# Kernel optimization log

Hardware: AMD Instinct MI355X
Metric: run time of the kernel (lower is better)

Reference implementation:

```python
import jax, jax.numpy as jnp
import numpy as np


def _square_distance(src, dst):
    # src: [B,N,C], dst: [B,M,C] -> [B,N,M] squared euclidean distances
    # ||s-d||^2 = -2 s.d + ||s||^2 + ||d||^2
    d = -2.0 * jnp.einsum('bnc,bmc->bnm', src, dst)
    d = d + jnp.sum(src * src, axis=-1)[:, :, None]
    d = d + jnp.sum(dst * dst, axis=-1)[:, None, :]
    return d


def setup_inputs() -> dict:
    key = jax.random.key(0)
    k1, k2 = jax.random.split(key)
    B, N, M, C = 8, 4096, 4096, 3
    f = jax.random.normal(k1, (B, N, C), dtype=jnp.float32)
    f_ = jax.random.normal(k2, (B, M, C), dtype=jnp.float32)
    return {"f": f, "f_": f_}


def reference(f, f_):
    dis = _square_distance(f, f_)          # [B,N,M]
    f2f_ = jnp.min(dis, axis=2)            # [B,N] nearest in f_ for each f point
    f_2f = jnp.min(dis, axis=1)            # [B,M] nearest in f for each f_ point
    d = jnp.mean(f2f_, axis=1) + jnp.mean(f_2f, axis=1)  # [B]
    return jnp.mean(d)
```

## Files before the change

### kernel.cpp

```cpp
#include <hip/hip_runtime.h>


typedef __attribute__((ext_vector_type(8))) short bf16x8;
typedef __attribute__((ext_vector_type(4))) float f32x4;

constexpr int B = 8;
constexpr int N = 4096;
constexpr int M = 4096;

constexpr int ROWS_PER_BLOCK = 128;
constexpr int SEG = 1024;
constexpr int SEGS = M / SEG;
constexpr int TILES = SEG / 16;

static __device__ __forceinline__ unsigned short f2bf(float v) {
    unsigned u = __float_as_uint(v);
    return (unsigned short)((u + 0x7FFFu + ((u >> 16) & 1u)) >> 16);
}
static __device__ __forceinline__ float bf2f(unsigned short b) {
    return __uint_as_float(((unsigned)b) << 16);
}
static __device__ __forceinline__ void split3(float v, unsigned short& a,
                                              unsigned short& b, unsigned short& c) {
    a = f2bf(v); float r = v - bf2f(a);
    b = f2bf(r); r -= bf2f(b);
    c = f2bf(r);
}

__global__ __launch_bounds__(256, 2) void chamfer_dir_mfma(
    const float* __restrict__ f,
    const float* __restrict__ f_,
    unsigned int* __restrict__ minA,
    unsigned int* __restrict__ minB)
{
    __shared__ bf16x8 Bt[TILES * 64];

    const int tid  = threadIdx.x;
    const int lane = tid & 63;
    const int w    = tid >> 6;
    const int r    = lane & 15;
    const int kg   = lane >> 4;

    const int dir = blockIdx.z;
    const int b   = blockIdx.y;
    const int rc  = blockIdx.x;

    const float* qsrc = dir ? f_ : f;
    const float* tsrc = dir ? f  : f_;
    unsigned int* omin = dir ? minB : minA;

    const int rowbase = rc * ROWS_PER_BLOCK + w * 32;
    bf16x8 afrag[2];
    #pragma unroll
    for (int rt = 0; rt < 2; ++rt) {
        const float* qp = qsrc + ((size_t)b * N + rowbase + rt * 16 + r) * 3;
        const float x = qp[0], y = qp[1], z = qp[2];
        unsigned short px0,px1,px2, py0,py1,py2, pz0,pz1,pz2, n0,n1,n2;
        split3(-2.f * x, px0, px1, px2);
        split3(-2.f * y, py0, py1, py2);
        split3(-2.f * z, pz0, pz1, pz2);
        split3(x*x + y*y + z*z, n0, n1, n2);
        const short ONE = 0x3F80;
        bf16x8 a;
        if (kg == 0)
            a = (bf16x8){(short)px0,(short)px0,(short)px1,(short)px1,(short)px0,(short)px2,(short)py0,(short)py0};
        else if (kg == 1)
            a = (bf16x8){(short)py1,(short)py1,(short)py0,(short)py2,(short)pz0,(short)pz0,(short)pz1,(short)pz1};
        else if (kg == 2)
            a = (bf16x8){(short)pz0,(short)pz2,(short)n0,(short)n1,(short)n2,ONE,ONE,ONE};
        else
            a = (bf16x8){0,0,0,0,0,0,0,0};
        afrag[rt] = a;
    }

    float rm[2][4];
    #pragma unroll
    for (int j = 0; j < 4; ++j) { rm[0][j] = 3.402823466e+38f; rm[1][j] = 3.402823466e+38f; }

    const float* tb = tsrc + (size_t)b * M * 3;
    const f32x4 zero = {0.f, 0.f, 0.f, 0.f};

    for (int s = 0; s < SEGS; ++s) {
        __syncthreads();
        #pragma unroll
        for (int i = 0; i < 4; ++i) {
            const int t = i * 256 + tid;
            const float* tp = tb + (size_t)(s * SEG + t) * 3;
            const float x = tp[0], y = tp[1], z = tp[2];
            unsigned short x0,x1,x2, y0,y1,y2, z0,z1,z2, m0,m1,m2;
            split3(x, x0, x1, x2);
            split3(y, y0, y1, y2);
            split3(z, z0, z1, z2);
            split3(x*x + y*y + z*z, m0, m1, m2);
            const short ONE = 0x3F80;
            const int tile = t >> 4, rr = t & 15;
            bf16x8* base = &Bt[tile * 64 + rr];
            base[ 0] = (bf16x8){(short)x0,(short)x1,(short)x0,(short)x1,(short)x2,(short)x0,(short)y0,(short)y1};
            base[16] = (bf16x8){(short)y0,(short)y1,(short)y2,(short)y0,(short)z0,(short)z1,(short)z0,(short)z1};
            base[32] = (bf16x8){(short)z2,(short)z0,ONE,ONE,ONE,(short)m0,(short)m1,(short)m2};
            base[48] = (bf16x8){0,0,0,0,0,0,0,0};
        }
        __syncthreads();

        bf16x8 bb = Bt[lane];
        #pragma unroll 4
        for (int ct = 0; ct < TILES; ++ct) {
            bf16x8 nb = Bt[((ct + 1) & (TILES - 1)) * 64 + lane];
            f32x4 c0 = __builtin_amdgcn_mfma_f32_16x16x32_bf16(afrag[0], bb, zero, 0, 0, 0);
            f32x4 c1 = __builtin_amdgcn_mfma_f32_16x16x32_bf16(afrag[1], bb, zero, 0, 0, 0);
            #pragma unroll
            for (int j = 0; j < 4; ++j) {
                rm[0][j] = fminf(rm[0][j], c0[j]);
                rm[1][j] = fminf(rm[1][j], c1[j]);
            }
            bb = nb;
        }
    }

    #pragma unroll
    for (int rt = 0; rt < 2; ++rt) {
        #pragma unroll
        for (int j = 0; j < 4; ++j) {
            float v = rm[rt][j];
            v = fminf(v, __shfl_xor(v, 1));
            v = fminf(v, __shfl_xor(v, 2));
            v = fminf(v, __shfl_xor(v, 4));
            v = fminf(v, __shfl_xor(v, 8));
            if (r == 0) {
                const int row = rowbase + rt * 16 + kg * 4 + j;
                atomicMin(&omin[b * N + row], __float_as_uint(v));
            }
        }
    }
}

__global__ __launch_bounds__(256) void reduce_out_kernel(
    const uint4* __restrict__ mins,
    float* __restrict__ out)
{
    __shared__ float wsum[4];
    const int tid = threadIdx.x;
    const uint4 v = mins[blockIdx.x * 256 + tid];
    float s = (__uint_as_float(v.x) + __uint_as_float(v.y))
            + (__uint_as_float(v.z) + __uint_as_float(v.w));

    #pragma unroll
    for (int off = 32; off > 0; off >>= 1) s += __shfl_down(s, off, 64);
    if ((tid & 63) == 0) wsum[tid >> 6] = s;
    __syncthreads();
    if (tid == 0) {
        const float r = (wsum[0] + wsum[1]) + (wsum[2] + wsum[3]);
        atomicAdd(out, r * (1.0f / 32768.0f));
    }
}

extern "C" void kernel_launch(void* const* d_in, const int* in_sizes, int n_in,
                              void* d_out, int out_size, void* d_ws, size_t ws_size,
                              hipStream_t stream) {
    (void)in_sizes; (void)n_in; (void)out_size; (void)ws_size;
    const float* f  = (const float*)d_in[0];
    const float* f_ = (const float*)d_in[1];
    float* out = (float*)d_out;

    unsigned int* minA = (unsigned int*)d_ws;
    unsigned int* minB = minA + (size_t)B * N;

    dim3 grid(N / ROWS_PER_BLOCK, B, 2);
    chamfer_dir_mfma<<<grid, 256, 0, stream>>>(f, f_, minA, minB);

    reduce_out_kernel<<<64, 256, 0, stream>>>((const uint4*)minA, out);
}
```

Before: 74.36 us.

## Precompute bf16 target fragments in a separate kernel and stream from global

Adds a prepass kernel that converts each target point into split-bf16 MFMA B-fragments once and stores them in workspace. The main kernel now reads these fragments straight from global memory, dropping the LDS staging and both per-segment barriers. It also splits the column range into four quarters per block, so the grid grows to 2048 blocks with a swizzled block index and higher occupancy. The trade-off is an extra launch, more global and L2 traffic for fragments, and four times as many atomicMin calls. Correctness depends on minA/minB being initialised elsewhere, as in the original code.

```diff
diff --git a/kernel.cpp b/kernel.cpp
--- a/kernel.cpp
+++ b/kernel.cpp
@@ -9,9 +9,9 @@
 constexpr int M = 4096;
 
 constexpr int ROWS_PER_BLOCK = 128;
-constexpr int SEG = 1024;
-constexpr int SEGS = M / SEG;
-constexpr int TILES = SEG / 16;
+constexpr int COLQ = 4;
+constexpr int CPB = M / COLQ;
+constexpr int TPB = CPB / 16;
 
 static __device__ __forceinline__ unsigned short f2bf(float v) {
     unsigned u = __float_as_uint(v);
@@ -27,13 +27,45 @@
     c = f2bf(r);
 }
 
-__global__ __launch_bounds__(256, 2) void chamfer_dir_mfma(
+__global__ __launch_bounds__(256) void make_frags(
     const float* __restrict__ f,
     const float* __restrict__ f_,
+    bf16x8* __restrict__ frag)
+{
+    const int gid = blockIdx.x * 256 + threadIdx.x;
+    const int dir = gid >> 15;
+    const int b   = (gid >> 12) & 7;
+    const int t   = gid & 4095;
+    const float* tsrc = dir ? f : f_;
+    const float* tp = tsrc + ((size_t)b * M + t) * 3;
+    const float x = tp[0], y = tp[1], z = tp[2];
+    unsigned short x0,x1,x2, y0,y1,y2, z0,z1,z2, m0,m1,m2;
+    split3(x, x0, x1, x2);
+    split3(y, y0, y1, y2);
+    split3(z, z0, z1, z2);
+    split3(x*x + y*y + z*z, m0, m1, m2);
+    const short ONE = 0x3F80;
+    const int tile = t >> 4, rr = t & 15;
+    bf16x8* base = frag + ((size_t)(dir * B + b) * 256 + tile) * 64 + rr;
+    base[ 0] = (bf16x8){(short)x0,(short)x1,(short)x0,(short)x1,(short)x2,(short)x0,(short)y0,(short)y1};
+    base[16] = (bf16x8){(short)y0,(short)y1,(short)y2,(short)y0,(short)z0,(short)z1,(short)z0,(short)z1};
+    base[32] = (bf16x8){(short)z2,(short)z0,ONE,ONE,ONE,(short)m0,(short)m1,(short)m2};
+    base[48] = (bf16x8){0,0,0,0,0,0,0,0};
+}
+
+__global__ __launch_bounds__(256, 6) void chamfer_dir_mfma(
+    const float* __restrict__ f,
+    const float* __restrict__ f_,
+    const bf16x8* __restrict__ frag,
     unsigned int* __restrict__ minA,
     unsigned int* __restrict__ minB)
 {
-    __shared__ bf16x8 Bt[TILES * 64];
+    const int bid = blockIdx.x;
+    const int swz = ((bid & 7) << 8) | (bid >> 3);
+    const int rc   = swz & 31;
+    const int cq   = (swz >> 5) & 3;
+    const int b    = (swz >> 7) & 7;
+    const int dir  = swz >> 10;
 
     const int tid  = threadIdx.x;
     const int lane = tid & 63;
@@ -41,12 +73,7 @@
     const int r    = lane & 15;
     const int kg   = lane >> 4;
 
-    const int dir = blockIdx.z;
-    const int b   = blockIdx.y;
-    const int rc  = blockIdx.x;
-
     const float* qsrc = dir ? f_ : f;
-    const float* tsrc = dir ? f  : f_;
     unsigned int* omin = dir ? minB : minA;
 
     const int rowbase = rc * ROWS_PER_BLOCK + w * 32;
@@ -77,44 +104,28 @@
     #pragma unroll
     for (int j = 0; j < 4; ++j) { rm[0][j] = 3.402823466e+38f; rm[1][j] = 3.402823466e+38f; }
 
-    const float* tb = tsrc + (size_t)b * M * 3;
+    const bf16x8* gf = frag + ((size_t)(dir * B + b) * 256 + cq * (TPB)) * 64;
     const f32x4 zero = {0.f, 0.f, 0.f, 0.f};
 
-    for (int s = 0; s < SEGS; ++s) {
-        __syncthreads();
+    bf16x8 bb0 = gf[lane];
+    bf16x8 bb1 = gf[64 + lane];
+    #pragma unroll 2
+    for (int it = 0; it < TPB / 2; ++it) {
+        bf16x8 nb0, nb1;
+        if (it + 1 < TPB / 2) {
+            nb0 = gf[(2 * it + 2) * 64 + lane];
+            nb1 = gf[(2 * it + 3) * 64 + lane];
+        }
+        f32x4 cA0 = __builtin_amdgcn_mfma_f32_16x16x32_bf16(afrag[0], bb0, zero, 0, 0, 0);
+        f32x4 cA1 = __builtin_amdgcn_mfma_f32_16x16x32_bf16(afrag[1], bb0, zero, 0, 0, 0);
+        f32x4 cB0 = __builtin_amdgcn_mfma_f32_16x16x32_bf16(afrag[0], bb1, zero, 0, 0, 0);
+        f32x4 cB1 = __builtin_amdgcn_mfma_f32_16x16x32_bf16(afrag[1], bb1, zero, 0, 0, 0);
         #pragma unroll
-        for (int i = 0; i < 4; ++i) {
-            const int t = i * 256 + tid;
-            const float* tp = tb + (size_t)(s * SEG + t) * 3;
-            const float x = tp[0], y = tp[1], z = tp[2];
-            unsigned short x0,x1,x2, y0,y1,y2, z0,z1,z2, m0,m1,m2;
-            split3(x, x0, x1, x2);
-            split3(y, y0, y1, y2);
-            split3(z, z0, z1, z2);
-            split3(x*x + y*y + z*z, m0, m1, m2);
-            const short ONE = 0x3F80;
-            const int tile = t >> 4, rr = t & 15;
-            bf16x8* base = &Bt[tile * 64 + rr];
-            base[ 0] = (bf16x8){(short)x0,(short)x1,(short)x0,(short)x1,(short)x2,(short)x0,(short)y0,(short)y1};
-            base[16] = (bf16x8){(short)y0,(short)y1,(short)y2,(short)y0,(short)z0,(short)z1,(short)z0,(short)z1};
-            base[32] = (bf16x8){(short)z2,(short)z0,ONE,ONE,ONE,(short)m0,(short)m1,(short)m2};
-            base[48] = (bf16x8){0,0,0,0,0,0,0,0};
+        for (int j = 0; j < 4; ++j) {
+            rm[0][j] = fminf(fminf(rm[0][j], cA0[j]), cB0[j]);
+            rm[1][j] = fminf(fminf(rm[1][j], cA1[j]), cB1[j]);
         }
-        __syncthreads();
-
-        bf16x8 bb = Bt[lane];
-        #pragma unroll 4
-        for (int ct = 0; ct < TILES; ++ct) {
-            bf16x8 nb = Bt[((ct + 1) & (TILES - 1)) * 64 + lane];
-            f32x4 c0 = __builtin_amdgcn_mfma_f32_16x16x32_bf16(afrag[0], bb, zero, 0, 0, 0);
-            f32x4 c1 = __builtin_amdgcn_mfma_f32_16x16x32_bf16(afrag[1], bb, zero, 0, 0, 0);
-            #pragma unroll
-            for (int j = 0; j < 4; ++j) {
-                rm[0][j] = fminf(rm[0][j], c0[j]);
-                rm[1][j] = fminf(rm[1][j], c1[j]);
-            }
-            bb = nb;
-        }
+        bb0 = nb0; bb1 = nb1;
     }
 
     #pragma unroll
@@ -164,9 +175,9 @@
 
     unsigned int* minA = (unsigned int*)d_ws;
     unsigned int* minB = minA + (size_t)B * N;
+    bf16x8* frag = (bf16x8*)((char*)d_ws + 256 * 1024);
 
-    dim3 grid(N / ROWS_PER_BLOCK, B, 2);
-    chamfer_dir_mfma<<<grid, 256, 0, stream>>>(f, f_, minA, minB);
-
+    make_frags<<<256, 256, 0, stream>>>(f, f_, frag);
+    chamfer_dir_mfma<<<2048, 256, 0, stream>>>(f, f_, frag, minA, minB);
     reduce_out_kernel<<<64, 256, 0, stream>>>((const uint4*)minA, out);
 }
```

New measurement: 83.22 us. +11.9%, slower.
